# Kernel tuning notes

Measured on AMD Instinct MI355X. Metric: run time of the kernel, lower is better.

## Reference

```python
import jax, jax.numpy as jnp
import numpy as np

REG = 5
SCORE_THRESH = 0.05
NMS_THRESH = 0.5
DET_PER_IMG = 100
BBOX_XFORM_CLIP = float(np.log(1000.0 / 16.0))
WEIGHTS = (10.0, 10.0, 5.0, 5.0, 10.0)  # (wx, wy, ww, wh, wa)
MAXV = 8  # max vertices of intersection of two convex quads


def decode(rel_codes, boxes):
    # rel_codes: [N, C*5], boxes: [N, 5] = (xc, yc, w, h, angle_deg)
    xc, yc, w, h, a = (boxes[:, i] for i in range(5))
    wx, wy, ww, wh, wa = WEIGHTS
    dx = rel_codes[:, 0::REG] / wx
    dy = rel_codes[:, 1::REG] / wy
    dw = jnp.minimum(rel_codes[:, 2::REG] / ww, BBOX_XFORM_CLIP)
    dh = jnp.minimum(rel_codes[:, 3::REG] / wh, BBOX_XFORM_CLIP)
    da = rel_codes[:, 4::REG] / wa
    px = dx * w[:, None] + xc[:, None]
    py = dy * h[:, None] + yc[:, None]
    pw = jnp.exp(dw) * w[:, None]
    ph = jnp.exp(dh) * h[:, None]
    pa = da * (180.0 / np.pi) + a[:, None]
    return jnp.stack([px, py, pw, ph, pa], axis=2).reshape(rel_codes.shape[0], -1)


def box_corners(b):
    # b: [..., 5] -> CCW corners [..., 4, 2]
    xc, yc, w, h, a = jnp.moveaxis(b, -1, 0)
    t = a * (np.pi / 180.0)
    c, s = jnp.cos(t), jnp.sin(t)
    lx = jnp.stack([-w, w, w, -w], -1) * 0.5
    ly = jnp.stack([-h, -h, h, h], -1) * 0.5
    x = xc[..., None] + lx * c[..., None] - ly * s[..., None]
    y = yc[..., None] + lx * s[..., None] + ly * c[..., None]
    return jnp.stack([x, y], -1)


def _clip_one(polyA, polyB):
    # Sutherland-Hodgman: clip quad A by CCW quad B; return intersection area.
    poly = jnp.zeros((MAXV, 2), polyA.dtype).at[:4].set(polyA)
    n0 = jnp.int32(4)
    idx = jnp.arange(MAXV)

    def clip_edge(carry, edge):
        poly, n = carry
        p1, p2 = edge[0], edge[1]
        valid = idx < n
        nxt = poly[jnp.where(idx + 1 < n, idx + 1, 0)]
        cur = poly
        e = p2 - p1
        sc = e[0] * (cur[:, 1] - p1[1]) - e[1] * (cur[:, 0] - p1[0])
        sn = e[0] * (nxt[:, 1] - p1[1]) - e[1] * (nxt[:, 0] - p1[0])
        in_c, in_n = sc >= 0, sn >= 0
        denom = sc - sn
        t = sc / jnp.where(jnp.abs(denom) > 1e-8, denom, 1.0)
        inter = cur + t[:, None] * (nxt - cur)
        emit_c = valid & in_c
        emit_i = valid & (in_c ^ in_n)
        pts = jnp.stack([cur, inter], 1).reshape(2 * MAXV, 2)
        flags = jnp.stack([emit_c, emit_i], 1).reshape(2 * MAXV)
        pos = jnp.where(flags, jnp.cumsum(flags) - 1, 2 * MAXV)
        newpoly = jnp.zeros((2 * MAXV + 1, 2), poly.dtype).at[pos].set(pts)[:MAXV]
        newn = jnp.minimum(jnp.sum(flags), MAXV).astype(jnp.int32)
        return (newpoly, newn), None

    edges = jnp.stack([polyB, jnp.roll(polyB, -1, axis=0)], 1)  # [4, 2, 2]
    (poly, n), _ = jax.lax.scan(clip_edge, (poly, n0), edges)
    valid = idx < n
    nxt = poly[jnp.where(idx + 1 < n, idx + 1, 0)]
    cross = poly[:, 0] * nxt[:, 1] - nxt[:, 0] * poly[:, 1]
    area = 0.5 * jnp.abs(jnp.sum(jnp.where(valid, cross, 0.0)))
    return jnp.where(n >= 3, area, 0.0)


def rotated_iou_matrix(boxes):
    # boxes: [N, 5] -> IoU [N, N]
    corners = box_corners(boxes)
    areas = boxes[:, 2] * boxes[:, 3]
    inter = jax.vmap(lambda ca: jax.vmap(lambda cb: _clip_one(ca, cb))(corners))(corners)
    union = areas[:, None] + areas[None, :] - inter
    return inter / jnp.maximum(union, 1e-8)


def greedy_nms(iou, valid):
    N = iou.shape[-1]
    ar = jnp.arange(N)

    def body(i, keep):
        sup = keep[i] & (iou[i] > NMS_THRESH) & (ar > i)
        return keep & ~sup

    keep = jax.lax.fori_loop(0, N, body, valid)
    return keep & (jnp.cumsum(keep) <= DET_PER_IMG)  # post_nms_top_n


def process_image(scores, proposals_dec):
    # scores: [N, C], proposals_dec: [N, C*5]; skip background class 0
    N, C = scores.shape
    fg = C - 1
    s = scores[:, 1:].T                                       # [fg, N]
    b = proposals_dec.reshape(N, C, REG)[:, 1:].transpose(1, 0, 2)  # [fg, N, 5]
    valid = s > SCORE_THRESH
    s_m = jnp.where(valid, s, -jnp.inf)
    order = jnp.argsort(-s_m, axis=1)                         # per-class descending sort
    s_sorted = jnp.take_along_axis(s_m, order, 1)
    b_sorted = jnp.take_along_axis(b, jnp.broadcast_to(order[:, :, None], b.shape), 1)
    v_sorted = jnp.take_along_axis(valid, order, 1)
    iou = jax.lax.stop_gradient(jax.vmap(rotated_iou_matrix)(b_sorted))  # [fg, N, N]
    keep = jax.vmap(greedy_nms)(iou, v_sorted)
    s_kept = jnp.where(keep, s_sorted, -jnp.inf)
    # cross-class top-k (limit to detections_per_img)
    top_s, top_idx = jax.lax.top_k(s_kept.reshape(-1), DET_PER_IMG)
    top_b = b_sorted.reshape(-1, REG)[top_idx]
    ok = jnp.isfinite(top_s)
    out = jnp.concatenate([top_b, top_s[:, None]], 1)         # (xc,yc,w,h,angle,score)
    return jnp.where(ok[:, None], out, 0.0)                   # [DET_PER_IMG, 6]


def setup_inputs() -> dict:
    key = jax.random.key(0)
    k1, k2, k3 = jax.random.split(key, 3)
    B, N, C = 2, 512, 16
    class_logits = jax.random.normal(k1, (B, N, C), jnp.float32)
    box_regression = jax.random.normal(k2, (B, N, C * REG), jnp.float32)
    u = jax.random.uniform(k3, (B, N, 5), jnp.float32)
    proposal_boxes = jnp.stack([
        u[..., 0] * 1024.0,          # xc
        u[..., 1] * 1024.0,          # yc
        16.0 + u[..., 2] * 240.0,    # w
        16.0 + u[..., 3] * 240.0,    # h
        u[..., 4] * 180.0 - 90.0,    # angle (deg)
    ], -1)
    return {"class_logits": class_logits, "box_regression": box_regression,
            "proposal_boxes": proposal_boxes}


def reference(class_logits, box_regression, proposal_boxes):
    B = class_logits.shape[0]
    probs = jax.nn.softmax(class_logits, -1)                  # [B, N, C]
    dec = jax.vmap(decode)(box_regression, proposal_boxes)    # [B, N, C*5]
    return jnp.stack([process_image(probs[i], dec[i]) for i in range(B)])  # [B, 100, 6]
```

## Files before the change

kernel.cpp:

```cpp
#include <hip/hip_runtime.h>

#define FG 15
#define NPROP 512
#define NCLS 16
#define NCI 30
#define SCORE_T 0.05f
#define NMS_T 0.5f
#define DETS 100
#define STRIPES 8
#define STAGE_CAP 4096

typedef unsigned long long u64;
typedef unsigned int u32;

__device__ __forceinline__ unsigned sortable_f32(float f) {
  unsigned u = __float_as_uint(f);
  return u ^ ((u >> 31) ? 0xFFFFFFFFu : 0x80000000u);
}

#define CLIP_EMIT(V, VALIDEXPR, CX, CY, NX, NY)                                \
  {                                                                            \
    bool valid = (VALIDEXPR);                                                  \
    float cx = (CX), cy = (CY), nx = (NX), ny = (NY);                          \
    float sc = ex * (cy - p1y) - ey * (cx - p1x);                              \
    float sn = ex * (ny - p1y) - ey * (nx - p1x);                              \
    bool ic = sc >= 0.f, inn = sn >= 0.f;                                      \
    float den = sc - sn;                                                       \
    float dsel = (fabsf(den) > 1e-8f) ? den : 1.f;                             \
    float tt = sc * __builtin_amdgcn_rcpf(dsel);                               \
    float qx = cx + tt * (nx - cx);                                            \
    float qy = cy + tt * (ny - cy);                                            \
    bool fC = valid && ic;                                                     \
    bool fI = valid && (ic != inn);                                            \
    _Pragma("unroll") for (int o = 0; o < 8; ++o) if (o <= 2 * (V)) {          \
      bool wr = fC && (m == o);                                                \
      ox[o] = wr ? cx : ox[o];                                                 \
      oy[o] = wr ? cy : oy[o];                                                 \
    }                                                                          \
    m += fC ? 1 : 0;                                                           \
    _Pragma("unroll") for (int o = 0; o < 8; ++o) if (o <= 2 * (V) + 1) {      \
      bool wr = fI && (m == o);                                                \
      ox[o] = wr ? qx : ox[o];                                                 \
      oy[o] = wr ? qy : oy[o];                                                 \
    }                                                                          \
    m += fI ? 1 : 0;                                                           \
  }

__device__ __forceinline__ float inter_area_fast(const float (&Ax)[4], const float (&Ay)[4],
                                                 const float (&Bx)[4], const float (&By)[4]) {
  float inx[8], iny[8];
  int n = 4;
#pragma unroll
  for (int v = 0; v < 4; ++v) {
    inx[v] = Ax[v]; iny[v] = Ay[v];
    inx[v + 4] = 0.f; iny[v + 4] = 0.f;
  }
#pragma unroll
  for (int e = 0; e < 4; ++e) {
    int e2 = (e + 1) & 3;
    float p1x = Bx[e], p1y = By[e];
    float ex = Bx[e2] - p1x, ey = By[e2] - p1y;
    float ox[8], oy[8];
    int m = 0;
#pragma unroll
    for (int o = 0; o < 8; ++o) { ox[o] = 0.f; oy[o] = 0.f; }
    if (e == 0) {
#pragma unroll
      for (int v = 0; v < 4; ++v) {
        CLIP_EMIT(v, true, inx[v], iny[v], inx[(v + 1) & 3], iny[(v + 1) & 3]);
      }
    } else {
#pragma unroll
      for (int v = 0; v < 8; ++v) {
        bool wrap = (v + 1 >= n);
        CLIP_EMIT(v, v < n, inx[v], iny[v],
                  wrap ? inx[0] : inx[(v + 1) & 7],
                  wrap ? iny[0] : iny[(v + 1) & 7]);
      }
    }
    n = (m < 8) ? m : 8;
#pragma unroll
    for (int o = 0; o < 8; ++o) { inx[o] = ox[o]; iny[o] = oy[o]; }
  }
  float s = 0.f;
#pragma unroll
  for (int v = 0; v < 8; ++v) {
    bool valid = v < n;
    bool wrap = (v + 1 >= n);
    float axx = inx[v], ayy = iny[v];
    float bxx = wrap ? inx[0] : inx[(v + 1) & 7];
    float byy = wrap ? iny[0] : iny[(v + 1) & 7];
    float cr = axx * byy - bxx * ayy;
    s += valid ? cr : 0.f;
  }
  float area = 0.5f * fabsf(s);
  return (n >= 3) ? area : 0.f;
}

__global__ void __launch_bounds__(512) k_pipe(
    const float* __restrict__ logits, const float* __restrict__ regr,
    const float* __restrict__ prop,
    float* __restrict__ ssort, float* __restrict__ bsort,
    u64* __restrict__ mask) {
  int ci = blockIdx.x;
  int s = blockIdx.y;
  int b = ci / FG, c = ci - b * FG + 1;
  int tid = threadIdx.x, lane = tid & 63, wv = tid >> 6;

  __shared__ __align__(16) u64 key2[NPROP + 8];
  __shared__ int rmap[NPROP];
  __shared__ int cnt[8];
  __shared__ __align__(16) float crn[NPROP][8];
  __shared__ float4 aabb[NPROP];
  __shared__ float areaL[NPROP];
  __shared__ u32 stage[STAGE_CAP];
  __shared__ int lcnt;

  if (tid == 0) lcnt = 0;

  float sc, bb[5];
  u64 k;
  {
#pragma clang fp contract(off)
    int g = b * NPROP + tid;
    const float* lg = logits + g * NCLS;
    float l[NCLS];
    float mx = -INFINITY;
#pragma unroll
    for (int q = 0; q < NCLS; ++q) { l[q] = lg[q]; mx = fmaxf(mx, l[q]); }
    float sum = 0.f, ec = 0.f;
#pragma unroll
    for (int q = 0; q < NCLS; ++q) {
      float e = expf(l[q] - mx);
      sum += e;
      if (q == c) ec = e;
    }
    sc = ec / sum;
    const float* pb = prop + g * 5;
    float xc = pb[0], yc = pb[1], w = pb[2], h = pb[3], a = pb[4];
    const float* r = regr + g * 80 + c * 5;
    float dx = r[0] / 10.0f;
    float dy = r[1] / 10.0f;
    float dw = fminf(r[2] / 5.0f, 4.135166556742356f);
    float dh = fminf(r[3] / 5.0f, 4.135166556742356f);
    float da = r[4] / 10.0f;
    bb[0] = dx * w + xc;
    bb[1] = dy * h + yc;
    bb[2] = expf(dw) * w;
    bb[3] = expf(dh) * h;
    bb[4] = da * 57.29577951308232f + a;
    float m = (sc > SCORE_T) ? sc : -INFINITY;
    k = ((u64)(~sortable_f32(m)) << 32) | (u32)tid;
  }
  bool val = sc > SCORE_T;
  u64 bal = __ballot(val);
  if (lane == 0) cnt[wv] = (int)__popcll(bal);
  __syncthreads();
  int base = 0, V = 0;
#pragma unroll
  for (int w = 0; w < 8; ++w) {
    int cw = cnt[w];
    base += (w < wv) ? cw : 0;
    V += cw;
  }
  if (val) key2[base + (int)__popcll(bal & ((1ull << lane) - 1ull))] = k;
  int Vpad = (V + 7) & ~7;
  if (tid < Vpad - V) key2[V + tid] = ~0ull;
  __syncthreads();

  if (tid < V) {
    u64 myk = key2[tid];
    int rank = 0;
    const ulonglong2* k2 = (const ulonglong2*)key2;
#pragma unroll 4
    for (int m = 0; m < Vpad / 2; ++m) {
      ulonglong2 kk = k2[m];
      rank += (kk.x < myk) ? 1 : 0;
      rank += (kk.y < myk) ? 1 : 0;
    }
    rmap[(int)(myk & 0xFFFFFFFFull)] = rank;
    if (s == 0) {
      u32 so = ~(u32)(myk >> 32);
      ssort[ci * NPROP + rank] = __uint_as_float(so ^ 0x80000000u);
    }
  }
  if (tid >= V && s == 0) ssort[ci * NPROP + tid] = -INFINITY;
  mask[((size_t)ci * NPROP + s + 8 * (tid >> 3)) * 8 + (tid & 7)] = 0ull;
  __syncthreads();

  if (val) {
    int r = rmap[tid];
    {
#pragma clang fp contract(off)
      float t = bb[4] * 0.017453292519943295f;
      float cs = cosf(t), sn = sinf(t);
      float hw = bb[2] * 0.5f, hh = bb[3] * 0.5f;
      float lx[4] = {-hw, hw, hw, -hw};
      float ly[4] = {-hh, -hh, hh, hh};
      float X[4], Y[4];
#pragma unroll
      for (int q = 0; q < 4; ++q) {
        X[q] = bb[0] + lx[q] * cs - ly[q] * sn;
        Y[q] = bb[1] + lx[q] * sn + ly[q] * cs;
      }
#pragma unroll
      for (int q = 0; q < 4; ++q) { crn[r][q] = X[q]; crn[r][4 + q] = Y[q]; }
      float xmn = fminf(fminf(X[0], X[1]), fminf(X[2], X[3]));
      float xmx = fmaxf(fmaxf(X[0], X[1]), fmaxf(X[2], X[3]));
      float ymn = fminf(fminf(Y[0], Y[1]), fminf(Y[2], Y[3]));
      float ymx = fmaxf(fmaxf(Y[0], Y[1]), fmaxf(Y[2], Y[3]));
      aabb[r] = make_float4(xmn, ymn, xmx, ymx);
      areaL[r] = bb[2] * bb[3];
      if (s == 0) {
        float* dst = bsort + ((size_t)ci * NPROP + r) * 5;
#pragma unroll
        for (int q = 0; q < 5; ++q) dst[q] = bb[q];
      }
    }
  }
  __syncthreads();

  for (int i = s; i < V; i += STRIPES) {
    float4 ai = aabb[i];
    float Ai = areaL[i];
    int j = (((i >> 6) << 6)) + tid;
    bool pass = false;
    if (j > i && j < V) {
      float4 aj = aabb[j];
      float ix = fminf(ai.z, aj.z) - fmaxf(ai.x, aj.x);
      float iy = fminf(ai.w, aj.w) - fmaxf(ai.y, aj.y);
      float ov = fmaxf(ix, 0.f) * fmaxf(iy, 0.f);
      pass = ov > 0.33f * (Ai + areaL[j]);
    }
    u64 bal2 = __ballot(pass);
    if (bal2) {
      int base2 = 0;
      if (lane == 0) base2 = atomicAdd(&lcnt, (int)__popcll(bal2));
      base2 = __shfl(base2, 0);
      if (pass) {
        int pos = base2 + (int)__popcll(bal2 & ((1ull << lane) - 1ull));
        if (pos < STAGE_CAP) stage[pos] = ((u32)i << 9) | (u32)j;
      }
    }
  }
  __syncthreads();
  int tot = lcnt < STAGE_CAP ? lcnt : STAGE_CAP;

  for (int p = tid; p < tot; p += 512) {
    u32 w = stage[p];
    int i = w >> 9, j = w & 511;
    float4 a0 = *(const float4*)&crn[i][0];
    float4 a1 = *(const float4*)&crn[i][4];
    float4 b0 = *(const float4*)&crn[j][0];
    float4 b1 = *(const float4*)&crn[j][4];
    float Ax[4] = {a0.x, a0.y, a0.z, a0.w};
    float Ay[4] = {a1.x, a1.y, a1.z, a1.w};
    float Bx[4] = {b0.x, b0.y, b0.z, b0.w};
    float By[4] = {b1.x, b1.y, b1.z, b1.w};
    float inter = inter_area_fast(Ax, Ay, Bx, By);
    float areaA = areaL[i];
    float areaB = areaL[j];
    float uni = (areaA + areaB) - inter;
    float iou = inter / fmaxf(uni, 1e-8f);
    if (iou > NMS_T)
      atomicOr(&mask[((size_t)ci * NPROP + i) * 8 + (j >> 6)], 1ull << (j & 63));
  }
}

__global__ void __launch_bounds__(256) k_nms(
    const float* __restrict__ ssort, const u64* __restrict__ mask,
    u64* __restrict__ kkey) {
  int ci = blockIdx.x;
  int b = ci / FG, cfg = ci - b * FG;
  __shared__ u64 lmask[(NPROP + 4) * 8];
  __shared__ u64 keptw[8];
  __shared__ int vcnt;
  __shared__ int wpre[8];
  int tid = threadIdx.x;
  const float* ss = ssort + ci * NPROP;
  if (tid == 0) vcnt = NPROP;
  __syncthreads();
  for (int i = tid; i < NPROP; i += 256)
    if (!(ss[i] > SCORE_T)) atomicMin(&vcnt, i);
  __syncthreads();
  int V = vcnt;
  for (int x = tid; x < V * 8; x += 256)
    lmask[x] = mask[(size_t)ci * NPROP * 8 + x];
  if (tid < 32) lmask[V * 8 + tid] = 0ull;
  __syncthreads();
  if (tid == 0) {
    u64 rem[8] = {0, 0, 0, 0, 0, 0, 0, 0};
    u64 kept[8] = {0, 0, 0, 0, 0, 0, 0, 0};
    u64 buf[4][8];
#pragma unroll
    for (int d = 0; d < 4; ++d)
#pragma unroll
      for (int w = 0; w < 8; ++w) buf[d][w] = lmask[d * 8 + w];
    int kc = 0;
    bool stop = (V == 0);
#pragma unroll
    for (int w8 = 0; w8 < 8; ++w8) {
      int lim = V - (w8 << 6);
      lim = lim > 64 ? 64 : lim;
      if (!stop && lim > 0) {
        int lim4 = (lim + 3) & ~3;
        for (int bp4 = 0; bp4 < lim4 && !stop; bp4 += 4) {
#pragma unroll
          for (int d = 0; d < 4; ++d) {
            int bp = bp4 + d;
            int i = (w8 << 6) | bp;
            if (bp < lim && !stop) {
              if (!((rem[w8] >> bp) & 1ull)) {
                kept[w8] |= 1ull << bp;
#pragma unroll
                for (int w = 0; w < 8; ++w) rem[w] |= buf[d][w];
                if (++kc >= DETS) stop = true;
              }
            }
#pragma unroll
            for (int w = 0; w < 8; ++w) buf[d][w] = lmask[(i + 4) * 8 + w];
          }
        }
      }
    }
#pragma unroll
    for (int w = 0; w < 8; ++w) keptw[w] = kept[w];
  }
  __syncthreads();
  if (tid == 0) {
    int acc = 0;
#pragma unroll
    for (int w = 0; w < 8; ++w) { wpre[w] = acc; acc += (int)__popcll(keptw[w]); }
  }
  __syncthreads();
  for (int i = tid; i < NPROP; i += 256) {
    u64 kw = keptw[i >> 6];
    if ((kw >> (i & 63)) & 1ull) {
      int rank = wpre[i >> 6] + (int)__popcll(kw & ((1ull << (i & 63)) - 1ull));
      float s = ss[i];
      u32 hi = __float_as_uint(s) ^ 0x80000000u;
      u32 flat = (u32)(cfg * NPROP + i);
      kkey[ci * 128 + rank] = ((u64)hi << 32) | (u32)(~flat);
    }
  }
  int total = wpre[7] + (int)__popcll(keptw[7]);
  for (int r = tid; r < 128; r += 256)
    if (r >= total) kkey[ci * 128 + r] = 0ull;
}

__global__ void __launch_bounds__(1024) k_topk(
    const u64* __restrict__ kkey,
    const float* __restrict__ bsort,
    float* __restrict__ out) {
  int b = blockIdx.x;
  __shared__ u64 lk[FG * 128];
  __shared__ u64 res[DETS];
  for (int x = threadIdx.x; x < FG * 128; x += 1024) lk[x] = kkey[b * FG * 128 + x];
  for (int x = threadIdx.x; x < DETS; x += 1024) res[x] = 0ull;
  __syncthreads();
  for (int x = threadIdx.x; x < FG * 128; x += 1024) {
    u64 key = lk[x];
    if (key == 0ull) continue;
    int rank = 0;
#pragma unroll
    for (int c = 0; c < FG; ++c) {
      const u64* a = &lk[c * 128];
      int pos = 0;
#pragma unroll
      for (int st = 64; st > 0; st >>= 1)
        pos += (a[pos + st - 1] > key) ? st : 0;
      rank += pos + ((a[pos] > key) ? 1 : 0);
    }
    if (rank < DETS) res[rank] = key;
  }
  __syncthreads();
  if (threadIdx.x < DETS) {
    u64 key = res[threadIdx.x];
    float* o = out + ((size_t)b * DETS + threadIdx.x) * 6;
    if (key == 0ull) {
#pragma unroll
      for (int q = 0; q < 6; ++q) o[q] = 0.f;
    } else {
      u32 flat = ~(u32)(key & 0xFFFFFFFFull);
      int cfg = flat >> 9, pos = flat & 511;
      const float* bx = bsort + (((size_t)b * FG + cfg) * NPROP + pos) * 5;
#pragma unroll
      for (int q = 0; q < 5; ++q) o[q] = bx[q];
      o[5] = __uint_as_float((u32)(key >> 32) ^ 0x80000000u);
    }
  }
}

extern "C" void kernel_launch(void* const* d_in, const int* in_sizes, int n_in,
                              void* d_out, int out_size, void* d_ws, size_t ws_size,
                              hipStream_t stream) {
  const float* logits = (const float*)d_in[0];
  const float* regr   = (const float*)d_in[1];
  const float* prop   = (const float*)d_in[2];
  float* out = (float*)d_out;

  float* ssort = (float*)d_ws;
  float* bsort = ssort + NCI * NPROP;
  u64* kkey    = (u64*)(bsort + NCI * NPROP * 5);
  u64* mask    = kkey + NCI * 128;

  hipLaunchKernelGGL(k_pipe, dim3(NCI, STRIPES), dim3(512), 0, stream,
                     logits, regr, prop, ssort, bsort, mask);
  hipLaunchKernelGGL(k_nms, dim3(NCI), dim3(256), 0, stream, ssort, mask, kkey);
  hipLaunchKernelGGL(k_topk, dim3(2), dim3(1024), 0, stream, kkey, bsort, out);
}
```

Before: 52.00 us.

## Fuse IoU, NMS and top-k into one kernel via last-block-done counters

Merges the three kernels into a single launch. Each block of a class atomically increments a counter, and the last of the 8 stripe blocks runs the greedy NMS using scores kept in shared memory. The last class block per image then does the top-k merge and writes the output. Shared memory is reused through one arena. This removes two kernel launch gaps and the global score round-trip, in exchange for a memset launch, extra fences, and serial tail work running on a single block.

```diff
diff --git a/kernel.cpp b/kernel.cpp
--- a/kernel.cpp
+++ b/kernel.cpp
@@ -97,24 +97,31 @@
   return (n >= 3) ? area : 0.f;
 }
 
-__global__ void __launch_bounds__(512) k_pipe(
+__global__ void __launch_bounds__(512) k_one(
     const float* __restrict__ logits, const float* __restrict__ regr,
     const float* __restrict__ prop,
-    float* __restrict__ ssort, float* __restrict__ bsort,
-    u64* __restrict__ mask) {
+    float* __restrict__ bsort,
+    u64* __restrict__ kkey,
+    u64* __restrict__ mask,
+    int* __restrict__ counters,
+    float* __restrict__ out) {
   int ci = blockIdx.x;
   int s = blockIdx.y;
   int b = ci / FG, c = ci - b * FG + 1;
   int tid = threadIdx.x, lane = tid & 63, wv = tid >> 6;
 
+  __shared__ __align__(16) char arena[43008];
+  u32* stage = (u32*)arena;
+  float* crn = (float*)(arena + 16384);
+  float4* aabb = (float4*)(arena + 32768);
+  float* areaL = (float*)(arena + 40960);
   __shared__ __align__(16) u64 key2[NPROP + 8];
+  __shared__ float ssl[NPROP];
   __shared__ int rmap[NPROP];
   __shared__ int cnt[8];
-  __shared__ __align__(16) float crn[NPROP][8];
-  __shared__ float4 aabb[NPROP];
-  __shared__ float areaL[NPROP];
-  __shared__ u32 stage[STAGE_CAP];
-  __shared__ int lcnt;
+  __shared__ u64 keptw[8];
+  __shared__ int wpre[8];
+  __shared__ int lcnt, bc1, bc2;
 
   if (tid == 0) lcnt = 0;
 
@@ -179,12 +186,9 @@
       rank += (kk.y < myk) ? 1 : 0;
     }
     rmap[(int)(myk & 0xFFFFFFFFull)] = rank;
-    if (s == 0) {
-      u32 so = ~(u32)(myk >> 32);
-      ssort[ci * NPROP + rank] = __uint_as_float(so ^ 0x80000000u);
-    }
-  }
-  if (tid >= V && s == 0) ssort[ci * NPROP + tid] = -INFINITY;
+    u32 so = ~(u32)(myk >> 32);
+    ssl[rank] = __uint_as_float(so ^ 0x80000000u);
+  }
   mask[((size_t)ci * NPROP + s + 8 * (tid >> 3)) * 8 + (tid & 7)] = 0ull;
   __syncthreads();
 
@@ -204,7 +208,7 @@
         Y[q] = bb[1] + lx[q] * sn + ly[q] * cs;
       }
 #pragma unroll
-      for (int q = 0; q < 4; ++q) { crn[r][q] = X[q]; crn[r][4 + q] = Y[q]; }
+      for (int q = 0; q < 4; ++q) { crn[r * 8 + q] = X[q]; crn[r * 8 + 4 + q] = Y[q]; }
       float xmn = fminf(fminf(X[0], X[1]), fminf(X[2], X[3]));
       float xmx = fmaxf(fmaxf(X[0], X[1]), fmaxf(X[2], X[3]));
       float ymn = fminf(fminf(Y[0], Y[1]), fminf(Y[2], Y[3]));
@@ -249,10 +253,10 @@
   for (int p = tid; p < tot; p += 512) {
     u32 w = stage[p];
     int i = w >> 9, j = w & 511;
-    float4 a0 = *(const float4*)&crn[i][0];
-    float4 a1 = *(const float4*)&crn[i][4];
-    float4 b0 = *(const float4*)&crn[j][0];
-    float4 b1 = *(const float4*)&crn[j][4];
+    float4 a0 = *(const float4*)&crn[i * 8];
+    float4 a1 = *(const float4*)&crn[i * 8 + 4];
+    float4 b0 = *(const float4*)&crn[j * 8];
+    float4 b1 = *(const float4*)&crn[j * 8 + 4];
     float Ax[4] = {a0.x, a0.y, a0.z, a0.w};
     float Ay[4] = {a1.x, a1.y, a1.z, a1.w};
     float Bx[4] = {b0.x, b0.y, b0.z, b0.w};
@@ -265,26 +269,17 @@
     if (iou > NMS_T)
       atomicOr(&mask[((size_t)ci * NPROP + i) * 8 + (j >> 6)], 1ull << (j & 63));
   }
-}
-
-__global__ void __launch_bounds__(256) k_nms(
-    const float* __restrict__ ssort, const u64* __restrict__ mask,
-    u64* __restrict__ kkey) {
-  int ci = blockIdx.x;
-  int b = ci / FG, cfg = ci - b * FG;
-  __shared__ u64 lmask[(NPROP + 4) * 8];
-  __shared__ u64 keptw[8];
-  __shared__ int vcnt;
-  __shared__ int wpre[8];
-  int tid = threadIdx.x;
-  const float* ss = ssort + ci * NPROP;
-  if (tid == 0) vcnt = NPROP;
-  __syncthreads();
-  for (int i = tid; i < NPROP; i += 256)
-    if (!(ss[i] > SCORE_T)) atomicMin(&vcnt, i);
-  __syncthreads();
-  int V = vcnt;
-  for (int x = tid; x < V * 8; x += 256)
+  __syncthreads();
+
+  __threadfence();
+  if (tid == 0) bc1 = atomicAdd(&counters[ci], 1);
+  __syncthreads();
+  if (bc1 != STRIPES - 1) return;
+
+  __threadfence();
+  u64* lmask = (u64*)arena;
+  __syncthreads();
+  for (int x = tid; x < V * 8; x += 512)
     lmask[x] = mask[(size_t)ci * NPROP * 8 + x];
   if (tid < 32) lmask[V * 8 + tid] = 0ull;
   __syncthreads();
@@ -325,46 +320,45 @@
     }
 #pragma unroll
     for (int w = 0; w < 8; ++w) keptw[w] = kept[w];
-  }
-  __syncthreads();
-  if (tid == 0) {
     int acc = 0;
 #pragma unroll
     for (int w = 0; w < 8; ++w) { wpre[w] = acc; acc += (int)__popcll(keptw[w]); }
   }
   __syncthreads();
-  for (int i = tid; i < NPROP; i += 256) {
+  {
+    int i = tid;
+    int cfg = c - 1;
     u64 kw = keptw[i >> 6];
     if ((kw >> (i & 63)) & 1ull) {
-      int rank = wpre[i >> 6] + (int)__popcll(kw & ((1ull << (i & 63)) - 1ull));
-      float s = ss[i];
-      u32 hi = __float_as_uint(s) ^ 0x80000000u;
+      int rk = wpre[i >> 6] + (int)__popcll(kw & ((1ull << (i & 63)) - 1ull));
+      float sv = ssl[i];
+      u32 hi = __float_as_uint(sv) ^ 0x80000000u;
       u32 flat = (u32)(cfg * NPROP + i);
-      kkey[ci * 128 + rank] = ((u64)hi << 32) | (u32)(~flat);
-    }
-  }
-  int total = wpre[7] + (int)__popcll(keptw[7]);
-  for (int r = tid; r < 128; r += 256)
-    if (r >= total) kkey[ci * 128 + r] = 0ull;
-}
-
-__global__ void __launch_bounds__(1024) k_topk(
-    const u64* __restrict__ kkey,
-    const float* __restrict__ bsort,
-    float* __restrict__ out) {
-  int b = blockIdx.x;
-  __shared__ u64 lk[FG * 128];
-  __shared__ u64 res[DETS];
-  for (int x = threadIdx.x; x < FG * 128; x += 1024) lk[x] = kkey[b * FG * 128 + x];
-  for (int x = threadIdx.x; x < DETS; x += 1024) res[x] = 0ull;
-  __syncthreads();
-  for (int x = threadIdx.x; x < FG * 128; x += 1024) {
+      kkey[ci * 128 + rk] = ((u64)hi << 32) | (u32)(~flat);
+    }
+    int total = wpre[7] + (int)__popcll(keptw[7]);
+    if (i < 128 && i >= total) kkey[ci * 128 + i] = 0ull;
+  }
+  __syncthreads();
+
+  __threadfence();
+  if (tid == 0) bc2 = atomicAdd(&counters[NCI + b], 1);
+  __syncthreads();
+  if (bc2 != FG - 1) return;
+
+  __threadfence();
+  u64* lk = (u64*)arena;
+  u64* res = (u64*)(arena + 16384);
+  for (int x = tid; x < FG * 128; x += 512) lk[x] = kkey[b * FG * 128 + x];
+  for (int x = tid; x < DETS; x += 512) res[x] = 0ull;
+  __syncthreads();
+  for (int x = tid; x < FG * 128; x += 512) {
     u64 key = lk[x];
     if (key == 0ull) continue;
     int rank = 0;
 #pragma unroll
-    for (int c = 0; c < FG; ++c) {
-      const u64* a = &lk[c * 128];
+    for (int cc = 0; cc < FG; ++cc) {
+      const u64* a = &lk[cc * 128];
       int pos = 0;
 #pragma unroll
       for (int st = 64; st > 0; st >>= 1)
@@ -374,9 +368,9 @@
     if (rank < DETS) res[rank] = key;
   }
   __syncthreads();
-  if (threadIdx.x < DETS) {
-    u64 key = res[threadIdx.x];
-    float* o = out + ((size_t)b * DETS + threadIdx.x) * 6;
+  if (tid < DETS) {
+    u64 key = res[tid];
+    float* o = out + ((size_t)b * DETS + tid) * 6;
     if (key == 0ull) {
 #pragma unroll
       for (int q = 0; q < 6; ++q) o[q] = 0.f;
@@ -399,13 +393,12 @@
   const float* prop   = (const float*)d_in[2];
   float* out = (float*)d_out;
 
-  float* ssort = (float*)d_ws;
-  float* bsort = ssort + NCI * NPROP;
+  float* bsort = (float*)d_ws;
   u64* kkey    = (u64*)(bsort + NCI * NPROP * 5);
   u64* mask    = kkey + NCI * 128;
-
-  hipLaunchKernelGGL(k_pipe, dim3(NCI, STRIPES), dim3(512), 0, stream,
-                     logits, regr, prop, ssort, bsort, mask);
-  hipLaunchKernelGGL(k_nms, dim3(NCI), dim3(256), 0, stream, ssort, mask, kkey);
-  hipLaunchKernelGGL(k_topk, dim3(2), dim3(1024), 0, stream, kkey, bsort, out);
+  int* counters = (int*)(mask + (size_t)NCI * NPROP * 8);
+
+  hipMemsetAsync(counters, 0, 32 * sizeof(int), stream);
+  hipLaunchKernelGGL(k_one, dim3(NCI, STRIPES), dim3(512), 0, stream,
+                     logits, regr, prop, bsort, kkey, mask, counters, out);
 }
```

Measured after the change: 92.49 us. +77.9%, slower.

## Use per-wave staging, shared-memory mask accumulation, and ballot-based valid count

Applied to the files above, without the earlier changes.

The candidate pair filter now gives each wave its own staging list, so it no longer needs a shared atomic counter. Each wave walks whole rows i across all chunks instead of all 512 threads sweeping a single row. IoU suppression bits are OR-ed into a shared-memory mask and written to global memory once, which replaces global atomics and the earlier zeroing pass. In the NMS kernel, the atomicMin scan that finds the valid count becomes a popcount over wave ballots, and one syncthreads is merged away. The cost is extra shared memory, a per-wave capacity limit that could drop pairs if exceeded, and possible load imbalance across waves.

```diff
diff --git a/kernel.cpp b/kernel.cpp
--- a/kernel.cpp
+++ b/kernel.cpp
@@ -8,7 +8,7 @@
 #define NMS_T 0.5f
 #define DETS 100
 #define STRIPES 8
-#define STAGE_CAP 4096
+#define WCAP 512
 
 typedef unsigned long long u64;
 typedef unsigned int u32;
@@ -113,10 +113,11 @@
   __shared__ __align__(16) float crn[NPROP][8];
   __shared__ float4 aabb[NPROP];
   __shared__ float areaL[NPROP];
-  __shared__ u32 stage[STAGE_CAP];
-  __shared__ int lcnt;
-
-  if (tid == 0) lcnt = 0;
+  __shared__ u32 stage[STRIPES][WCAP];
+  __shared__ int wcnts[8];
+  __shared__ u64 lmask2[NPROP];
+
+  lmask2[tid] = 0ull;
 
   float sc, bb[5];
   u64 k;
@@ -185,7 +186,6 @@
     }
   }
   if (tid >= V && s == 0) ssort[ci * NPROP + tid] = -INFINITY;
-  mask[((size_t)ci * NPROP + s + 8 * (tid >> 3)) * 8 + (tid & 7)] = 0ull;
   __syncthreads();
 
   if (val) {
@@ -220,51 +220,77 @@
   }
   __syncthreads();
 
-  for (int i = s; i < V; i += STRIPES) {
-    float4 ai = aabb[i];
-    float Ai = areaL[i];
-    int j = (((i >> 6) << 6)) + tid;
-    bool pass = false;
-    if (j > i && j < V) {
-      float4 aj = aabb[j];
-      float ix = fminf(ai.z, aj.z) - fmaxf(ai.x, aj.x);
-      float iy = fminf(ai.w, aj.w) - fmaxf(ai.y, aj.y);
-      float ov = fmaxf(ix, 0.f) * fmaxf(iy, 0.f);
-      pass = ov > 0.33f * (Ai + areaL[j]);
-    }
-    u64 bal2 = __ballot(pass);
-    if (bal2) {
-      int base2 = 0;
-      if (lane == 0) base2 = atomicAdd(&lcnt, (int)__popcll(bal2));
-      base2 = __shfl(base2, 0);
-      if (pass) {
-        int pos = base2 + (int)__popcll(bal2 & ((1ull << lane) - 1ull));
-        if (pos < STAGE_CAP) stage[pos] = ((u32)i << 9) | (u32)j;
-      }
-    }
-  }
-  __syncthreads();
-  int tot = lcnt < STAGE_CAP ? lcnt : STAGE_CAP;
-
-  for (int p = tid; p < tot; p += 512) {
-    u32 w = stage[p];
-    int i = w >> 9, j = w & 511;
-    float4 a0 = *(const float4*)&crn[i][0];
-    float4 a1 = *(const float4*)&crn[i][4];
-    float4 b0 = *(const float4*)&crn[j][0];
-    float4 b1 = *(const float4*)&crn[j][4];
-    float Ax[4] = {a0.x, a0.y, a0.z, a0.w};
-    float Ay[4] = {a1.x, a1.y, a1.z, a1.w};
-    float Bx[4] = {b0.x, b0.y, b0.z, b0.w};
-    float By[4] = {b1.x, b1.y, b1.z, b1.w};
-    float inter = inter_area_fast(Ax, Ay, Bx, By);
-    float areaA = areaL[i];
-    float areaB = areaL[j];
-    float uni = (areaA + areaB) - inter;
-    float iou = inter / fmaxf(uni, 1e-8f);
-    if (iou > NMS_T)
-      atomicOr(&mask[((size_t)ci * NPROP + i) * 8 + (j >> 6)], 1ull << (j & 63));
-  }
+  {
+    int nch = (V + 63) >> 6;
+    int wcnt = 0;
+    for (int t = wv;; t += 8) {
+      int i = s + 8 * t;
+      if (i >= V) break;
+      float4 ai = aabb[i];
+      float Ai = areaL[i];
+      for (int ch = i >> 6; ch < nch; ++ch) {
+        int j = (ch << 6) | lane;
+        bool pass = false;
+        if (j > i && j < V) {
+          float4 aj = aabb[j];
+          float ix = fminf(ai.z, aj.z) - fmaxf(ai.x, aj.x);
+          float iy = fminf(ai.w, aj.w) - fmaxf(ai.y, aj.y);
+          float ov = fmaxf(ix, 0.f) * fmaxf(iy, 0.f);
+          pass = ov > 0.33f * (Ai + areaL[j]);
+        }
+        u64 bal2 = __ballot(pass);
+        if (pass) {
+          int pos = wcnt + (int)__popcll(bal2 & ((1ull << lane) - 1ull));
+          if (pos < WCAP) stage[wv][pos] = ((u32)i << 9) | (u32)j;
+        }
+        wcnt += (int)__popcll(bal2);
+      }
+    }
+    if (lane == 0) wcnts[wv] = wcnt < WCAP ? wcnt : WCAP;
+  }
+  __syncthreads();
+
+  {
+    int c0 = wcnts[0], c1 = wcnts[1], c2 = wcnts[2], c3 = wcnts[3];
+    int c4 = wcnts[4], c5 = wcnts[5], c6 = wcnts[6], c7 = wcnts[7];
+    int p1 = c0, p2 = p1 + c1, p3 = p2 + c2, p4 = p3 + c3;
+    int p5 = p4 + c4, p6 = p5 + c5, p7 = p6 + c6;
+    int total = p7 + c7;
+    for (int p = tid; p < total; p += 512) {
+      int r = (p >= p1) + (p >= p2) + (p >= p3) + (p >= p4) +
+              (p >= p5) + (p >= p6) + (p >= p7);
+      u32 w = 0;
+      switch (r) {
+        case 0: w = stage[0][p]; break;
+        case 1: w = stage[1][p - p1]; break;
+        case 2: w = stage[2][p - p2]; break;
+        case 3: w = stage[3][p - p3]; break;
+        case 4: w = stage[4][p - p4]; break;
+        case 5: w = stage[5][p - p5]; break;
+        case 6: w = stage[6][p - p6]; break;
+        default: w = stage[7][p - p7]; break;
+      }
+      int i = w >> 9, j = w & 511;
+      float4 a0 = *(const float4*)&crn[i][0];
+      float4 a1 = *(const float4*)&crn[i][4];
+      float4 b0 = *(const float4*)&crn[j][0];
+      float4 b1 = *(const float4*)&crn[j][4];
+      float Ax[4] = {a0.x, a0.y, a0.z, a0.w};
+      float Ay[4] = {a1.x, a1.y, a1.z, a1.w};
+      float Bx[4] = {b0.x, b0.y, b0.z, b0.w};
+      float By[4] = {b1.x, b1.y, b1.z, b1.w};
+      float inter = inter_area_fast(Ax, Ay, Bx, By);
+      float areaA = areaL[i];
+      float areaB = areaL[j];
+      float uni = (areaA + areaB) - inter;
+      float iou = inter / fmaxf(uni, 1e-8f);
+      if (iou > NMS_T)
+        atomicOr(&lmask2[(((i - s) >> 3) << 3) | (j >> 6)], 1ull << (j & 63));
+    }
+  }
+  __syncthreads();
+
+  mask[((size_t)ci * NPROP + s + 8 * (tid >> 3)) * 8 + (tid & 7)] = lmask2[tid];
 }
 
 __global__ void __launch_bounds__(256) k_nms(
@@ -274,16 +300,18 @@
   int b = ci / FG, cfg = ci - b * FG;
   __shared__ u64 lmask[(NPROP + 4) * 8];
   __shared__ u64 keptw[8];
-  __shared__ int vcnt;
+  __shared__ int vcnt8[8];
   __shared__ int wpre[8];
-  int tid = threadIdx.x;
+  int tid = threadIdx.x, lane = tid & 63, wv = tid >> 6;
   const float* ss = ssort + ci * NPROP;
-  if (tid == 0) vcnt = NPROP;
-  __syncthreads();
-  for (int i = tid; i < NPROP; i += 256)
-    if (!(ss[i] > SCORE_T)) atomicMin(&vcnt, i);
-  __syncthreads();
-  int V = vcnt;
+  for (int chunk = wv; chunk < 8; chunk += 4) {
+    u64 bal = __ballot(ss[(chunk << 6) | lane] > SCORE_T);
+    if (lane == 0) vcnt8[chunk] = (int)__popcll(bal);
+  }
+  __syncthreads();
+  int V = 0;
+#pragma unroll
+  for (int w = 0; w < 8; ++w) V += vcnt8[w];
   for (int x = tid; x < V * 8; x += 256)
     lmask[x] = mask[(size_t)ci * NPROP * 8 + x];
   if (tid < 32) lmask[V * 8 + tid] = 0ull;
@@ -325,9 +353,6 @@
     }
 #pragma unroll
     for (int w = 0; w < 8; ++w) keptw[w] = kept[w];
-  }
-  __syncthreads();
-  if (tid == 0) {
     int acc = 0;
 #pragma unroll
     for (int w = 0; w < 8; ++w) { wpre[w] = acc; acc += (int)__popcll(keptw[w]); }
```

Result: faster. 45.55 us (-12.4%).
